# Kernel tuning notes

Hardware: AMD Instinct MI355X
Metric: run time of the kernel (lower is better)

The kernel has to match this reference:

```python
import jax, jax.numpy as jnp
import numpy as np

H = 16          # num_heads
DK = 64         # k_dim_head
DV = 64         # v_dim_head
DIM = 1024      # model dim (= H*DK = H*DV)


def _split_heads(x, h):
    # ... T (H d) -> ... H T d
    x = x.reshape(x.shape[:-1] + (h, -1))
    return jnp.swapaxes(x, -2, -3)


def _merge_heads(x):
    # ... H T d -> ... T (H d)
    x = jnp.swapaxes(x, -2, -3)
    return x.reshape(x.shape[:-2] + (-1,))


def setup_inputs() -> dict:
    key = jax.random.key(0)
    ks = jax.random.split(key, 8)
    B, T = 2, 2048
    q = jax.random.normal(ks[0], (B, T, DIM), dtype=jnp.float32)
    k = jax.random.normal(ks[1], (B, T, DIM), dtype=jnp.float32)
    v = jax.random.normal(ks[2], (B, T, DIM), dtype=jnp.float32)
    # causal boolean mask [T, T] (True = attend)
    mask = jnp.tril(jnp.ones((T, T), dtype=bool))
    s = 1.0 / np.sqrt(DIM)
    # weights stored as [in, out] so projection is x @ W (== torch Linear, no bias)
    Wq = jax.random.normal(ks[3], (DIM, H * DK), dtype=jnp.float32) * s
    Wk = jax.random.normal(ks[4], (DIM, H * DK), dtype=jnp.float32) * s
    Wv = jax.random.normal(ks[5], (DIM, H * DV), dtype=jnp.float32) * s
    Wo = jax.random.normal(ks[6], (H * DV, DIM), dtype=jnp.float32) * s
    return {"q": q, "k": k, "v": v, "mask": mask,
            "Wq": Wq, "Wk": Wk, "Wv": Wv, "Wo": Wo}


def reference(q, k, v, mask, Wq, Wk, Wv, Wo):
    q_i = _split_heads(q @ Wq, H)                       # ... H T dk
    k_i = _split_heads(k @ Wk, H)                       # ... H T dk
    v_i = _split_heads(v @ Wv, H)                       # ... H T dv
    s_qk = jnp.einsum('...hik,...hjk->...hij', q_i, k_i) / jnp.sqrt(
        jnp.asarray(DK, dtype=q_i.dtype))               # ... H T T
    neg = -jnp.finfo(s_qk.dtype).max
    s_qk = jnp.where(mask, s_qk, neg)
    attn = jax.nn.softmax(s_qk, axis=-1)
    vals = jnp.einsum('...hij,...hjv->...hiv', attn, v_i)
    return _merge_heads(vals) @ Wo                      # ... T out_dim
```

## Files before the change

kernel.cpp:

```cpp
#include <hip/hip_runtime.h>
#include <hip/hip_bf16.h>
#include <stdint.h>

#define T_SEQ  2048
#define DMODEL 1024
#define NBATCH 2
#define NHEAD  16
#define DHEAD  64
#define MTOT   (NBATCH * T_SEQ)

typedef __attribute__((ext_vector_type(8))) short short8_t;
typedef __attribute__((ext_vector_type(4))) float f32x4;
typedef __attribute__((ext_vector_type(16))) float f32x16;
typedef __attribute__((ext_vector_type(2))) __bf16 bhalf2_t;
typedef __attribute__((ext_vector_type(4))) uint32_t uint4_t;

typedef const __attribute__((address_space(1))) void* gas_t;
typedef __attribute__((address_space(3))) void* las_t;

__device__ __forceinline__ ushort f2bf(float f) {
    return __builtin_bit_cast(unsigned short, (__bf16)f);
}
__device__ __forceinline__ uint32_t pk_bf16(float a, float b) {
    bhalf2_t t; t[0] = (__bf16)a; t[1] = (__bf16)b;
    return __builtin_bit_cast(uint32_t, t);
}

template <int B>
__device__ __forceinline__ short8_t pack8(const f32x16 &s) {
    uint4_t u;
    u[0] = pk_bf16(s[B + 0], s[B + 1]);
    u[1] = pk_bf16(s[B + 2], s[B + 3]);
    u[2] = pk_bf16(s[B + 4], s[B + 5]);
    u[3] = pk_bf16(s[B + 6], s[B + 7]);
    return __builtin_bit_cast(short8_t, u);
}

__global__ __launch_bounds__(256) void convert_qkv_kernel(
        const float* __restrict__ q, const float* __restrict__ k,
        const float* __restrict__ v, ushort* __restrict__ outb) {
    const size_t per = (size_t)MTOT * DMODEL / 4;
    size_t idx = (size_t)blockIdx.x * 256 + threadIdx.x;
    int t = (int)(idx / per);
    size_t i = idx - (size_t)t * per;
    const float4* src = (const float4*)(t == 0 ? q : (t == 1 ? k : v));
    float4 val = src[i];
    uint2 o;
    o.x = pk_bf16(val.x, val.y);
    o.y = pk_bf16(val.z, val.w);
    ((uint2*)outb)[(size_t)t * per + i] = o;
}

__global__ __launch_bounds__(256) void convw_kernel(
        const float* __restrict__ Wq, const float* __restrict__ Wk,
        const float* __restrict__ Wv, const float* __restrict__ Wo,
        ushort* __restrict__ wt) {
    __shared__ float tile[32][33];
    int z = blockIdx.z;
    const float* W = z == 0 ? Wq : z == 1 ? Wk : z == 2 ? Wv : Wo;
    const float sc = (z == 0) ? 0.18033688011f : 1.0f;
    ushort* out = wt + (size_t)z * DMODEL * DMODEL;
    int tx = threadIdx.x, ty = threadIdx.y;
    int k0 = blockIdx.x * 32, n0 = blockIdx.y * 32;
    #pragma unroll
    for (int i = 0; i < 4; i++)
        tile[ty + i * 8][tx] = W[(size_t)(k0 + ty + i * 8) * DMODEL + n0 + tx];
    __syncthreads();
    #pragma unroll
    for (int i = 0; i < 4; i++)
        out[(size_t)(n0 + ty + i * 8) * DMODEL + k0 + tx] = f2bf(tile[tx][ty + i * 8] * sc);
}

template <bool OUT_F32>
__global__ __launch_bounds__(256, 2) void gemm_bt_kernel(
        const ushort* __restrict__ Aall, const ushort* __restrict__ Btall,
        void* __restrict__ Call, int M, int N, int K) {
    const ushort* A  = Aall  + (size_t)blockIdx.z * M * K;
    const ushort* Bt = Btall + (size_t)blockIdx.z * N * K;

    __shared__ ushort As[128 * 32];
    __shared__ ushort Bs[128 * 32];

    const int tid  = threadIdx.x;
    const int lane = tid & 63;
    const int wid  = tid >> 6;
    const int wr = wid >> 1, wc = wid & 1;
    const int m_base = blockIdx.x * 128;
    const int n_base = blockIdx.y * 128;

    f32x4 acc[4][4] = {};

    const int srow = lane >> 2;
    const int scol = (lane & 3) * 8;

    for (int kk = 0; kk < K; kk += 32) {
        __syncthreads();
        #pragma unroll
        for (int i = 0; i < 2; i++) {
            int c = wid * 2 + i;
            const ushort* ga = A  + (size_t)(m_base + c * 16 + srow) * K + kk + scol;
            const ushort* gb = Bt + (size_t)(n_base + c * 16 + srow) * K + kk + scol;
            __builtin_amdgcn_global_load_lds((gas_t)ga, (las_t)(As + c * 512), 16, 0, 0);
            __builtin_amdgcn_global_load_lds((gas_t)gb, (las_t)(Bs + c * 512), 16, 0, 0);
        }
        __syncthreads();
        short8_t a[4], b[4];
        #pragma unroll
        for (int mt = 0; mt < 4; mt++)
            a[mt] = *(const short8_t*)(As + (wr * 64 + mt * 16 + (lane & 15)) * 32 + (lane >> 4) * 8);
        #pragma unroll
        for (int nt = 0; nt < 4; nt++)
            b[nt] = *(const short8_t*)(Bs + (wc * 64 + nt * 16 + (lane & 15)) * 32 + (lane >> 4) * 8);
        #pragma unroll
        for (int mt = 0; mt < 4; mt++)
            #pragma unroll
            for (int nt = 0; nt < 4; nt++)
                acc[mt][nt] = __builtin_amdgcn_mfma_f32_16x16x32_bf16(a[mt], b[nt], acc[mt][nt], 0, 0, 0);
    }

    const int row0 = m_base + wr * 64 + (lane >> 4) * 4;
    const int col0 = n_base + wc * 64 + (lane & 15);
    if constexpr (OUT_F32) {
        float* C = (float*)Call + (size_t)blockIdx.z * M * N;
        #pragma unroll
        for (int mt = 0; mt < 4; mt++)
            #pragma unroll
            for (int nt = 0; nt < 4; nt++)
                #pragma unroll
                for (int r = 0; r < 4; r++)
                    C[(size_t)(row0 + mt * 16 + r) * N + col0 + nt * 16] = acc[mt][nt][r];
    } else {
        ushort* C = (ushort*)Call + (size_t)blockIdx.z * M * N;
        #pragma unroll
        for (int mt = 0; mt < 4; mt++)
            #pragma unroll
            for (int nt = 0; nt < 4; nt++)
                #pragma unroll
                for (int r = 0; r < 4; r++)
                    C[(size_t)(row0 + mt * 16 + r) * N + col0 + nt * 16] = f2bf(acc[mt][nt][r]);
    }
}

__global__ __launch_bounds__(64, 2) void attn_kernel(
        const ushort* __restrict__ Qp, const ushort* __restrict__ Kp,
        const ushort* __restrict__ Vp, ushort* __restrict__ Op) {
    __shared__ __attribute__((aligned(16))) ushort Ksh[64 * 72];
    __shared__ __attribute__((aligned(16))) ushort Vts[64 * 72];

    const int lane = threadIdx.x;
    const int m31 = lane & 31, hi = lane >> 5;

    const int id = (int)blockIdx.x;
    const int low = id & 255, k8 = id >> 8;
    const int bh = low >> 3;
    const int u = ((k8 >> 1) << 3) | (low & 7);
    const int qb = (k8 & 1) ? 63 - u : u;
    const int b = bh >> 4, h = bh & 15;

    const ushort* Qb = Qp + (size_t)(b * T_SEQ) * DMODEL + h * DHEAD;
    const ushort* Kb = Kp + (size_t)(b * T_SEQ) * DMODEL + h * DHEAD;
    const ushort* Vb = Vp + (size_t)(b * T_SEQ) * DMODEL + h * DHEAD;
    ushort* Ob = Op + (size_t)(b * T_SEQ) * DMODEL + h * DHEAD;

    const int nt = (qb >> 1) + 1;
    const int q0w = qb * 32;
    const int qg = q0w + m31;

    const int kr8 = lane >> 3, kc8 = (lane & 7) * 8;
    const int kvp = lane & 31, dvh = lane >> 5;
    const int lp = kvp & 7, q2 = lp >> 1;
    const int q2p = ((q2 & 1) << 1) | (q2 >> 1);
    const int kvc = (kvp & ~7) | (q2p << 1) | (lp & 1);

    short8_t kreg[8], vreg[8];
    auto LOADKV = [&](int kv0) {
        #pragma unroll
        for (int i = 0; i < 8; i++)
            kreg[i] = *(const short8_t*)(Kb + (size_t)(kv0 + kr8 + 8 * i) * DMODEL + kc8);
        const ushort* vsrc = Vb + (size_t)(kv0 + 2 * kvp) * DMODEL + dvh * 32;
        #pragma unroll
        for (int j = 0; j < 4; j++) {
            vreg[j]     = *(const short8_t*)(vsrc + j * 8);
            vreg[4 + j] = *(const short8_t*)(vsrc + DMODEL + j * 8);
        }
    };
    auto WRITEKV = [&]() {
        #pragma unroll
        for (int i = 0; i < 8; i++)
            *(short8_t*)(&Ksh[(kr8 + 8 * i) * 72 + kc8]) = kreg[i];
        #pragma unroll
        for (int j = 0; j < 4; j++) {
            uint4_t a = __builtin_bit_cast(uint4_t, vreg[j]);
            uint4_t o = __builtin_bit_cast(uint4_t, vreg[4 + j]);
            #pragma unroll
            for (int jj = 0; jj < 4; jj++) {
                int d0 = dvh * 32 + j * 8 + 2 * jj;
                *(uint32_t*)(&Vts[(d0 + 0) * 72 + kvc * 2]) =
                    __builtin_amdgcn_perm(o[jj], a[jj], 0x05040100u);
                *(uint32_t*)(&Vts[(d0 + 1) * 72 + kvc * 2]) =
                    __builtin_amdgcn_perm(o[jj], a[jj], 0x07060302u);
            }
        }
    };

    short8_t qf[4];
    #pragma unroll
    for (int dkc = 0; dkc < 4; dkc++)
        qf[dkc] = *(const short8_t*)(Qb + (size_t)(q0w + m31) * DMODEL + dkc * 16 + hi * 8);

    f32x16 acc0 = {}, acc1 = {};
    float mrun = -1e30f, lrun = 0.f;

    LOADKV(0);
    WRITEKV();

    for (int t = 0; t < nt; ++t) {
        const int kv0 = t * 64;
        const bool need_mask = (t == nt - 1);

        if (t + 1 < nt) LOADKV((t + 1) * 64);

        f32x16 s0 = {}, s1 = {};
        __builtin_amdgcn_s_setprio(1);
        #pragma unroll
        for (int dkc = 0; dkc < 4; dkc++) {
            short8_t kf0 = *(const short8_t*)(&Ksh[(m31) * 72 + dkc * 16 + hi * 8]);
            short8_t kf1 = *(const short8_t*)(&Ksh[(32 + m31) * 72 + dkc * 16 + hi * 8]);
            s0 = __builtin_amdgcn_mfma_f32_32x32x16_bf16(kf0, qf[dkc], s0, 0, 0, 0);
            s1 = __builtin_amdgcn_mfma_f32_32x32x16_bf16(kf1, qf[dkc], s1, 0, 0, 0);
        }
        __builtin_amdgcn_s_setprio(0);

        if (need_mask) {
            const int kvb = kv0 + 4 * hi;
            #pragma unroll
            for (int r = 0; r < 16; r++) {
                int kvl = (r & 3) + 8 * (r >> 2);
                if (kvb + kvl      > qg) s0[r] = -1e30f;
                if (kvb + kvl + 32 > qg) s1[r] = -1e30f;
            }
        }

        float tm[16];
        #pragma unroll
        for (int r = 0; r < 16; r++) tm[r] = fmaxf(s0[r], s1[r]);
        #pragma unroll
        for (int st = 8; st >= 1; st >>= 1)
            #pragma unroll
            for (int i = 0; i < st; i++) tm[i] = fmaxf(tm[i], tm[i + st]);
        float pmax = fmaxf(tm[0], __shfl_xor(tm[0], 32));

        if (!__all(pmax <= mrun + 8.f)) {
            float mnew = fmaxf(mrun, pmax);
            float fac = exp2f(mrun - mnew);
            mrun = mnew;
            lrun *= fac;
            #pragma unroll
            for (int r = 0; r < 16; r++) {
                float fr = __shfl(fac, (r & 3) + 8 * (r >> 2) + 4 * hi);
                acc0[r] *= fr; acc1[r] *= fr;
            }
        }

        float ps[16];
        #pragma unroll
        for (int r = 0; r < 16; r++) {
            s0[r] = exp2f(s0[r] - mrun);
            s1[r] = exp2f(s1[r] - mrun);
            ps[r] = s0[r] + s1[r];
        }
        #pragma unroll
        for (int st = 8; st >= 1; st >>= 1)
            #pragma unroll
            for (int i = 0; i < st; i++) ps[i] += ps[i + st];
        lrun += ps[0] + __shfl_xor(ps[0], 32);

        short8_t pa[4];
        pa[0] = pack8<0>(s0);
        pa[1] = pack8<8>(s0);
        pa[2] = pack8<0>(s1);
        pa[3] = pack8<8>(s1);
        __builtin_amdgcn_s_setprio(1);
        #pragma unroll
        for (int ks = 0; ks < 4; ks++) {
            short8_t vf0 = *(const short8_t*)(&Vts[(m31) * 72 + ks * 16 + hi * 8]);
            short8_t vf1 = *(const short8_t*)(&Vts[(32 + m31) * 72 + ks * 16 + hi * 8]);
            acc0 = __builtin_amdgcn_mfma_f32_32x32x16_bf16(pa[ks], vf0, acc0, 0, 0, 0);
            acc1 = __builtin_amdgcn_mfma_f32_32x32x16_bf16(pa[ks], vf1, acc1, 0, 0, 0);
        }
        __builtin_amdgcn_s_setprio(0);

        if (t + 1 < nt) WRITEKV();
    }

    float linv = __builtin_amdgcn_rcpf(lrun);
    #pragma unroll
    for (int r = 0; r < 16; r++) {
        int ql = (r & 3) + 8 * (r >> 2) + 4 * hi;
        float li = __shfl(linv, ql);
        ushort* orow = Ob + (size_t)(q0w + ql) * DMODEL + m31;
        orow[0]  = f2bf(acc0[r] * li);
        orow[32] = f2bf(acc1[r] * li);
    }
}

extern "C" void kernel_launch(void* const* d_in, const int* in_sizes, int n_in,
                              void* d_out, int out_size, void* d_ws, size_t ws_size,
                              hipStream_t stream) {
    (void)in_sizes; (void)n_in; (void)out_size; (void)ws_size;
    const float* q  = (const float*)d_in[0];
    const float* k  = (const float*)d_in[1];
    const float* v  = (const float*)d_in[2];
    const float* Wq = (const float*)d_in[4];
    const float* Wk = (const float*)d_in[5];
    const float* Wv = (const float*)d_in[6];
    const float* Wo = (const float*)d_in[7];

    ushort* ws = (ushort*)d_ws;
    const size_t MK = (size_t)MTOT * DMODEL;
    const size_t NK = (size_t)DMODEL * DMODEL;
    ushort* qkvb = ws;
    ushort* wt   = ws + 3 * MK;
    ushort* qkvp = ws + 3 * MK + 4 * NK;
    ushort* Op   = ws;

    convert_qkv_kernel<<<dim3(12288), dim3(256), 0, stream>>>(q, k, v, qkvb);
    convw_kernel<<<dim3(32, 32, 4), dim3(32, 8), 0, stream>>>(Wq, Wk, Wv, Wo, wt);
    gemm_bt_kernel<false><<<dim3(32, 8, 3), dim3(256), 0, stream>>>(qkvb, wt, (void*)qkvp,
                                                                    MTOT, DMODEL, DMODEL);
    attn_kernel<<<dim3(2048), dim3(64), 0, stream>>>(qkvp, qkvp + MK, qkvp + 2 * MK, Op);
    gemm_bt_kernel<true><<<dim3(32, 8, 1), dim3(256), 0, stream>>>(Op, wt + 3 * NK, d_out,
                                                                   MTOT, DMODEL, DMODEL);
}
```

Baseline: 148.1 us.

## Pair causal query blocks per workgroup and stream K via direct-to-LDS loads

Each workgroup now handles two query blocks, u and 63-u, in one loop of 33 KV tiles. This balances causal work per block and halves the grid. K tiles are loaded straight into an XOR-swizzled, unpadded LDS buffer with global_load_lds, and manual vmcnt waits pipeline them against compute. V loads are moved so the next tile's load is issued before the PV MFMAs. The change is meant to remove the register round-trip for K and the triangular load imbalance across blocks, but it has no barriers (a single wave, which is fine) and drops occupancy to launch_bounds(64,1).

```diff
diff --git a/kernel.cpp b/kernel.cpp
--- a/kernel.cpp
+++ b/kernel.cpp
@@ -141,20 +141,16 @@
     }
 }
 
-__global__ __launch_bounds__(64, 2) void attn_kernel(
+__global__ __launch_bounds__(64, 1) void attn_kernel(
         const ushort* __restrict__ Qp, const ushort* __restrict__ Kp,
         const ushort* __restrict__ Vp, ushort* __restrict__ Op) {
-    __shared__ __attribute__((aligned(16))) ushort Ksh[64 * 72];
+    __shared__ __attribute__((aligned(16))) ushort Ksh[64 * 64];
     __shared__ __attribute__((aligned(16))) ushort Vts[64 * 72];
 
     const int lane = threadIdx.x;
     const int m31 = lane & 31, hi = lane >> 5;
-
-    const int id = (int)blockIdx.x;
-    const int low = id & 255, k8 = id >> 8;
-    const int bh = low >> 3;
-    const int u = ((k8 >> 1) << 3) | (low & 7);
-    const int qb = (k8 & 1) ? 63 - u : u;
+    const int bx = (int)blockIdx.x;
+    const int u = bx & 31, bh = bx >> 5;
     const int b = bh >> 4, h = bh & 15;
 
     const ushort* Qb = Qp + (size_t)(b * T_SEQ) * DMODEL + h * DHEAD;
@@ -162,21 +158,26 @@
     const ushort* Vb = Vp + (size_t)(b * T_SEQ) * DMODEL + h * DHEAD;
     ushort* Ob = Op + (size_t)(b * T_SEQ) * DMODEL + h * DHEAD;
 
-    const int nt = (qb >> 1) + 1;
-    const int q0w = qb * 32;
-    const int qg = q0w + m31;
-
-    const int kr8 = lane >> 3, kc8 = (lane & 7) * 8;
+    const int na = (u >> 1) + 1;
+
+    const int krow = lane >> 3;
+    const int kchunk = (lane & 7) ^ krow;
+    auto ISSUE_K = [&](int kv0) {
+        #pragma unroll
+        for (int i = 0; i < 8; i++)
+            __builtin_amdgcn_global_load_lds(
+                (gas_t)(Kb + (size_t)(kv0 + 8 * i + krow) * DMODEL + kchunk * 8),
+                (las_t)(Ksh + i * 512), 16, 0, 0);
+    };
+    const int kx = m31 & 7;
+
     const int kvp = lane & 31, dvh = lane >> 5;
     const int lp = kvp & 7, q2 = lp >> 1;
     const int q2p = ((q2 & 1) << 1) | (q2 >> 1);
     const int kvc = (kvp & ~7) | (q2p << 1) | (lp & 1);
 
-    short8_t kreg[8], vreg[8];
-    auto LOADKV = [&](int kv0) {
-        #pragma unroll
-        for (int i = 0; i < 8; i++)
-            kreg[i] = *(const short8_t*)(Kb + (size_t)(kv0 + kr8 + 8 * i) * DMODEL + kc8);
+    short8_t vreg[8];
+    auto LOADV = [&](int kv0) {
         const ushort* vsrc = Vb + (size_t)(kv0 + 2 * kvp) * DMODEL + dvh * 32;
         #pragma unroll
         for (int j = 0; j < 4; j++) {
@@ -184,10 +185,7 @@
             vreg[4 + j] = *(const short8_t*)(vsrc + DMODEL + j * 8);
         }
     };
-    auto WRITEKV = [&]() {
-        #pragma unroll
-        for (int i = 0; i < 8; i++)
-            *(short8_t*)(&Ksh[(kr8 + 8 * i) * 72 + kc8]) = kreg[i];
+    auto WRITEV = [&]() {
         #pragma unroll
         for (int j = 0; j < 4; j++) {
             uint4_t a = __builtin_bit_cast(uint4_t, vreg[j]);
@@ -203,6 +201,8 @@
         }
     };
 
+    int qb = u;
+    int q0w = qb * 32, qg = q0w + m31;
     short8_t qf[4];
     #pragma unroll
     for (int dkc = 0; dkc < 4; dkc++)
@@ -211,25 +211,53 @@
     f32x16 acc0 = {}, acc1 = {};
     float mrun = -1e30f, lrun = 0.f;
 
-    LOADKV(0);
-    WRITEKV();
-
-    for (int t = 0; t < nt; ++t) {
+    auto WRITE_O = [&]() {
+        float linv = __builtin_amdgcn_rcpf(lrun);
+        #pragma unroll
+        for (int r = 0; r < 16; r++) {
+            int ql = (r & 3) + 8 * (r >> 2) + 4 * hi;
+            float li = __shfl(linv, ql);
+            ushort* orow = Ob + (size_t)(q0w + ql) * DMODEL + m31;
+            orow[0]  = f2bf(acc0[r] * li);
+            orow[32] = f2bf(acc1[r] * li);
+        }
+    };
+    auto TILE = [&](int t) { return (t < na) ? t : t - na; };
+
+    ISSUE_K(TILE(0) * 64);
+    LOADV(TILE(0) * 64);
+
+    for (int tt = 0; tt < 33; ++tt) {
+        if (tt == na) {
+            WRITE_O();
+            acc0 = f32x16{}; acc1 = f32x16{};
+            mrun = -1e30f; lrun = 0.f;
+            qb = 63 - u; q0w = qb * 32; qg = q0w + m31;
+            #pragma unroll
+            for (int dkc = 0; dkc < 4; dkc++)
+                qf[dkc] = *(const short8_t*)(Qb + (size_t)(q0w + m31) * DMODEL + dkc * 16 + hi * 8);
+            asm volatile("s_waitcnt vmcnt(0)" ::: "memory");
+            __builtin_amdgcn_sched_barrier(0);
+        }
+        const int t = TILE(tt);
         const int kv0 = t * 64;
-        const bool need_mask = (t == nt - 1);
-
-        if (t + 1 < nt) LOADKV((t + 1) * 64);
+        const bool need_mask = (t == (qb >> 1));
+
+        asm volatile("s_waitcnt vmcnt(8)" ::: "memory");
+        __builtin_amdgcn_sched_barrier(0);
 
         f32x16 s0 = {}, s1 = {};
         __builtin_amdgcn_s_setprio(1);
         #pragma unroll
         for (int dkc = 0; dkc < 4; dkc++) {
-            short8_t kf0 = *(const short8_t*)(&Ksh[(m31) * 72 + dkc * 16 + hi * 8]);
-            short8_t kf1 = *(const short8_t*)(&Ksh[(32 + m31) * 72 + dkc * 16 + hi * 8]);
+            short8_t kf0 = *(const short8_t*)(&Ksh[(m31) * 64 + (((dkc << 1) | hi) ^ kx) * 8]);
+            short8_t kf1 = *(const short8_t*)(&Ksh[(32 + m31) * 64 + (((dkc << 1) | hi) ^ kx) * 8]);
             s0 = __builtin_amdgcn_mfma_f32_32x32x16_bf16(kf0, qf[dkc], s0, 0, 0, 0);
             s1 = __builtin_amdgcn_mfma_f32_32x32x16_bf16(kf1, qf[dkc], s1, 0, 0, 0);
         }
         __builtin_amdgcn_s_setprio(0);
+
+        if (tt + 1 < 33) ISSUE_K(TILE(tt + 1) * 64);
 
         if (need_mask) {
             const int kvb = kv0 + 4 * hi;
@@ -240,7 +268,6 @@
                 if (kvb + kvl + 32 > qg) s1[r] = -1e30f;
             }
         }
-
         float tm[16];
         #pragma unroll
         for (int r = 0; r < 16; r++) tm[r] = fmaxf(s0[r], s1[r]);
@@ -261,7 +288,6 @@
                 acc0[r] *= fr; acc1[r] *= fr;
             }
         }
-
         float ps[16];
         #pragma unroll
         for (int r = 0; r < 16; r++) {
@@ -274,6 +300,13 @@
             #pragma unroll
             for (int i = 0; i < st; i++) ps[i] += ps[i + st];
         lrun += ps[0] + __shfl_xor(ps[0], 32);
+
+        if (tt == 32) { asm volatile("s_waitcnt vmcnt(0)" ::: "memory"); }
+        else          { asm volatile("s_waitcnt vmcnt(8)" ::: "memory"); }
+        __builtin_amdgcn_sched_barrier(0);
+        WRITEV();
+
+        if (tt + 1 < 33) LOADV(TILE(tt + 1) * 64);
 
         short8_t pa[4];
         pa[0] = pack8<0>(s0);
@@ -289,19 +322,8 @@
             acc1 = __builtin_amdgcn_mfma_f32_32x32x16_bf16(pa[ks], vf1, acc1, 0, 0, 0);
         }
         __builtin_amdgcn_s_setprio(0);
-
-        if (t + 1 < nt) WRITEKV();
     }
-
-    float linv = __builtin_amdgcn_rcpf(lrun);
-    #pragma unroll
-    for (int r = 0; r < 16; r++) {
-        int ql = (r & 3) + 8 * (r >> 2) + 4 * hi;
-        float li = __shfl(linv, ql);
-        ushort* orow = Ob + (size_t)(q0w + ql) * DMODEL + m31;
-        orow[0]  = f2bf(acc0[r] * li);
-        orow[32] = f2bf(acc1[r] * li);
-    }
+    WRITE_O();
 }
 
 extern "C" void kernel_launch(void* const* d_in, const int* in_sizes, int n_in,
@@ -328,7 +350,7 @@
     convw_kernel<<<dim3(32, 32, 4), dim3(32, 8), 0, stream>>>(Wq, Wk, Wv, Wo, wt);
     gemm_bt_kernel<false><<<dim3(32, 8, 3), dim3(256), 0, stream>>>(qkvb, wt, (void*)qkvp,
                                                                     MTOT, DMODEL, DMODEL);
-    attn_kernel<<<dim3(2048), dim3(64), 0, stream>>>(qkvp, qkvp + MK, qkvp + 2 * MK, Op);
+    attn_kernel<<<dim3(1024), dim3(64), 0, stream>>>(qkvp, qkvp + MK, qkvp + 2 * MK, Op);
     gemm_bt_kernel<true><<<dim3(32, 8, 1), dim3(256), 0, stream>>>(Op, wt + 3 * NK, d_out,
                                                                    MTOT, DMODEL, DMODEL);
 }
```

Result: slower. 165.1 us (+11.5%).
